# Kernel optimization log

Hardware: AMD Instinct MI355X
Metric: run time of the kernel (lower is better)

The kernel has to match this reference:

```python
import jax, jax.numpy as jnp
import numpy as np

N_NODES = 100000
N_EDGES = 800000
N_DIM = 2
HID = 128
EPS = 1e-12  # torch F.normalize eps


def setup_inputs() -> dict:
    key = jax.random.key(0)
    ks = jax.random.split(key, 12)
    x = jax.random.normal(ks[0], (N_NODES, N_DIM), dtype=jnp.float32)
    v = jax.random.normal(ks[1], (N_NODES, N_DIM), dtype=jnp.float32)
    src = jax.random.randint(ks[2], (N_EDGES,), 0, N_NODES, dtype=jnp.int32)
    dst = jax.random.randint(ks[3], (N_EDGES,), 0, N_NODES, dtype=jnp.int32)
    # fNN parameters, stored as [in, out] (y = h @ W + b, equivalent to torch Linear)
    def lin(k, fan_in, fan_out):
        bound = 1.0 / np.sqrt(fan_in)
        kw, kb = jax.random.split(k)
        W = jax.random.uniform(kw, (fan_in, fan_out), jnp.float32, -bound, bound)
        b = jax.random.uniform(kb, (fan_out,), jnp.float32, -bound, bound)
        return W, b
    W0, b0 = lin(ks[4], 1, HID)
    W1, b1 = lin(ks[5], HID, HID)
    W2, b2 = lin(ks[6], HID, HID)
    W3, b3 = lin(ks[7], HID, 1)
    gamma = jnp.float32(0.1)
    return {"x": x, "v": v, "src": src, "dst": dst, "gamma": gamma,
            "W0": W0, "b0": b0, "W1": W1, "b1": b1,
            "W2": W2, "b2": b2, "W3": W3, "b3": b3}


def reference(x, v, src, dst, gamma, W0, b0, W1, b1, W2, b2, W3, b3):
    n_nodes = x.shape[0]
    # per-edge displacement: dst position - src position (non-periodic euclid)
    dr = x[dst] - x[src]                                  # [E, N_dim]
    abs_dr = jnp.linalg.norm(dr, axis=-1, keepdims=True)  # [E, 1]
    unit_dr = dr / jnp.maximum(abs_dr, EPS)               # F.normalize
    # small MLP on scalar distance: 1 -> 128 -> 128 -> 128 -> 1, ReLU between
    h = jax.nn.relu(abs_dr @ W0 + b0)
    h = jax.nn.relu(h @ W1 + b1)
    h = jax.nn.relu(h @ W2 + b2)
    force = h @ W3 + b3                                   # [E, 1]
    msg = force * unit_dr                                 # [E, N_dim]
    # scatter-sum messages onto destination nodes
    sum_force = jax.ops.segment_sum(msg, dst, num_segments=n_nodes)  # [N, N_dim]
    # acceleration = aggregated force - gamma * velocity
    return sum_force - gamma * v
```

## Files before the change

kernel.cpp:

```cpp
#include <hip/hip_runtime.h>
#include <math.h>


#define M_TAB 2048
#define INV_MTAB (1.0f / 2048.0f)
#define EPSF 1e-12f
#define RANGE_N 2048
#define RSHIFT 11
#define NBUCK 64
#define P_SL 8
#define BCHUNK 2048
#define TPTS 4
#define NTABB (M_TAB / TPTS)
#define MAXRUN 64
#define SRC_BITS 17
#define SRC_MASK 0x1FFFFu

__device__ __forceinline__ void build_table4(
    int base, int tid, const float* __restrict__ W0,
    const float* __restrict__ b0, const float* __restrict__ W1,
    const float* __restrict__ b1, const float* __restrict__ W2,
    const float* __restrict__ b2, const float* __restrict__ W3,
    const float* __restrict__ b3, float* __restrict__ table,
    float* bufA, float* bufB) {
  const int j = tid;
  if (j < 128) {
    float w = W0[j], b = b0[j];
#pragma unroll
    for (int p = 0; p < TPTS; ++p) {
      float u = (float)(base + p) * INV_MTAB;
      float dd = u / (1.f - u);
      bufA[j * TPTS + p] = fmaxf(fmaf(dd, w, b), 0.f);
    }
  }
  __syncthreads();
  float acc[TPTS];
  if (j < 128) {
    float b = b1[j];
#pragma unroll
    for (int p = 0; p < TPTS; ++p) acc[p] = b;
#pragma unroll 8
    for (int k = 0; k < 128; ++k) {
      float w = W1[k * 128 + j];
      float4 h = *(const float4*)&bufA[k * TPTS];
      acc[0] = fmaf(h.x, w, acc[0]);
      acc[1] = fmaf(h.y, w, acc[1]);
      acc[2] = fmaf(h.z, w, acc[2]);
      acc[3] = fmaf(h.w, w, acc[3]);
    }
  }
  __syncthreads();
  if (j < 128) {
#pragma unroll
    for (int p = 0; p < TPTS; ++p) bufB[j * TPTS + p] = fmaxf(acc[p], 0.f);
  }
  __syncthreads();
  if (j < 128) {
    float b = b2[j];
#pragma unroll
    for (int p = 0; p < TPTS; ++p) acc[p] = b;
#pragma unroll 8
    for (int k = 0; k < 128; ++k) {
      float w = W2[k * 128 + j];
      float4 h = *(const float4*)&bufB[k * TPTS];
      acc[0] = fmaf(h.x, w, acc[0]);
      acc[1] = fmaf(h.y, w, acc[1]);
      acc[2] = fmaf(h.z, w, acc[2]);
      acc[3] = fmaf(h.w, w, acc[3]);
    }
    float w3 = W3[j];
#pragma unroll
    for (int p = 0; p < TPTS; ++p) bufA[j * TPTS + p] = fmaxf(acc[p], 0.f) * w3;
  }
  __syncthreads();
  for (int s = 64; s > 0; s >>= 1) {
    if (j < s) {
#pragma unroll
      for (int p = 0; p < TPTS; ++p)
        bufA[j * TPTS + p] += bufA[(j + s) * TPTS + p];
    }
    __syncthreads();
  }
  if (j < TPTS) table[base + j] = bufA[j] + b3[0];
}

__global__ __launch_bounds__(256) void kbin(
    const int* __restrict__ src, const int* __restrict__ dst,
    const float* __restrict__ W0, const float* __restrict__ b0,
    const float* __restrict__ W1, const float* __restrict__ b1,
    const float* __restrict__ W2, const float* __restrict__ b2,
    const float* __restrict__ W3, const float* __restrict__ b3,
    unsigned* __restrict__ binData, int* __restrict__ cntTab,
    int* __restrict__ offTab, float* __restrict__ table, int E, int NB) {
  __shared__ float smem[1024];
  __shared__ int cntL[NBUCK];
  __shared__ int offL[NBUCK];
  const int tid = threadIdx.x;
  const int bid = blockIdx.x;

  if (bid < NTABB) {
    build_table4(bid * TPTS, tid, W0, b0, W1, b1, W2, b2, W3, b3, table,
                 smem, smem + 512);
    return;
  }
  const int b = bid - NTABB;
  if (tid < NBUCK) cntL[tid] = 0;
  __syncthreads();
  const int e0 = b * BCHUNK + tid * 8;
  int mdst[8], msrc[8], mrank[8];
  if (e0 + 7 < E) {
    int4 c0 = *(const int4*)(dst + e0);
    int4 c1 = *(const int4*)(dst + e0 + 4);
    int4 a0 = *(const int4*)(src + e0);
    int4 a1 = *(const int4*)(src + e0 + 4);
    mdst[0] = c0.x; mdst[1] = c0.y; mdst[2] = c0.z; mdst[3] = c0.w;
    mdst[4] = c1.x; mdst[5] = c1.y; mdst[6] = c1.z; mdst[7] = c1.w;
    msrc[0] = a0.x; msrc[1] = a0.y; msrc[2] = a0.z; msrc[3] = a0.w;
    msrc[4] = a1.x; msrc[5] = a1.y; msrc[6] = a1.z; msrc[7] = a1.w;
  } else {
#pragma unroll
    for (int i = 0; i < 8; ++i) {
      bool vv = (e0 + i < E);
      msrc[i] = vv ? src[e0 + i] : 0;
      mdst[i] = vv ? dst[e0 + i] : -1;
    }
  }
#pragma unroll
  for (int i = 0; i < 8; ++i)
    if (mdst[i] >= 0) mrank[i] = atomicAdd(&cntL[mdst[i] >> RSHIFT], 1);
  __syncthreads();
  if (tid == 0) {
    int s = 0;
#pragma unroll
    for (int k = 0; k < NBUCK; ++k) {
      offL[k] = s;
      s += cntL[k];
    }
  }
  __syncthreads();
  if (tid < NBUCK) {
    cntTab[b * NBUCK + tid] = cntL[tid];
    offTab[b * NBUCK + tid] = offL[tid];
  }
  unsigned* gout = binData + (size_t)b * BCHUNK;
#pragma unroll
  for (int i = 0; i < 8; ++i) {
    if (mdst[i] >= 0) {
      int pos = offL[mdst[i] >> RSHIFT] + mrank[i];
      gout[pos] = ((unsigned)(mdst[i] & (RANGE_N - 1)) << SRC_BITS) |
                  (unsigned)msrc[i];
    }
  }
}

__global__ __launch_bounds__(512) void kcons(
    const unsigned* __restrict__ binData, const int* __restrict__ cntTab,
    const int* __restrict__ offTab, const float* __restrict__ table,
    const float* __restrict__ x, float* __restrict__ partial, int NB,
    int n_nodes, int n_out) {
  __shared__ float acc[RANGE_N * 2];
  __shared__ float2 xl[RANGE_N];
  __shared__ int runStart[MAXRUN];
  __shared__ int pref[MAXRUN + 1];
  const int tid = threadIdx.x;
  const int p = blockIdx.x & (P_SL - 1);
  const int r = blockIdx.x >> 3;
  const int node0 = r * RANGE_N;

  for (int i = tid; i < RANGE_N * 2; i += 512) acc[i] = 0.f;
  for (int i = tid; i < RANGE_N; i += 512)
    xl[i] = (node0 + i < n_nodes) ? ((const float2*)x)[node0 + i]
                                  : make_float2(0.f, 0.f);
  const int nrun = (NB - p + P_SL - 1) / P_SL;
  for (int j = tid; j < nrun; j += 512) {
    int b = p + j * P_SL;
    runStart[j] = b * BCHUNK + offTab[b * NBUCK + r];
    pref[j + 1] = cntTab[b * NBUCK + r];
  }
  __syncthreads();
  if (tid == 0) {
    pref[0] = 0;
    for (int j = 0; j < nrun; ++j) pref[j + 1] += pref[j];
  }
  __syncthreads();

  const int T = pref[nrun];
  for (int g = tid; g < T; g += 512) {
    int lo = 0, hi = nrun;
    while (hi - lo > 1) {
      int mid = (lo + hi) >> 1;
      if (pref[mid] <= g) lo = mid; else hi = mid;
    }
    unsigned ent = binData[(size_t)runStart[lo] + (g - pref[lo])];
    int dloc = (int)(ent >> SRC_BITS);
    int s = (int)(ent & SRC_MASK);
    float2 xs = ((const float2*)x)[s];
    float2 xt = xl[dloc];
    float dx = xt.x - xs.x, dy = xt.y - xs.y;
    float d = sqrtf(fmaf(dx, dx, dy * dy));
    float u = d / (1.f + d);
    float idxf = u * (float)M_TAB;
    int i0 = (int)idxf;
    if (i0 > M_TAB - 2) i0 = M_TAB - 2;
    float frac = idxf - (float)i0;
    float f0 = table[i0], f1 = table[i0 + 1];
    float f = fmaf(frac, f1 - f0, f0);
    float sc = f / fmaxf(d, EPSF);
    atomicAdd(&acc[dloc * 2], sc * dx);
    atomicAdd(&acc[dloc * 2 + 1], sc * dy);
  }
  __syncthreads();

  const int cnt2 = min(RANGE_N, n_nodes - node0);
  float2* po = (float2*)(partial + (size_t)p * n_out) + node0;
  const float2* a2 = (const float2*)acc;
  for (int i = tid; i < cnt2; i += 512) po[i] = a2[i];
}

__global__ __launch_bounds__(256) void k4_finish(
    const float4* __restrict__ v4, const float* __restrict__ gamma,
    const float4* __restrict__ part4, float4* __restrict__ out4, int n4) {
  int i = blockIdx.x * blockDim.x + threadIdx.x;
  if (i >= n4) return;
  float g = -gamma[0];
  float4 a = v4[i];
  float4 acc = make_float4(g * a.x, g * a.y, g * a.z, g * a.w);
#pragma unroll
  for (int c = 0; c < P_SL; ++c) {
    float4 p = part4[(size_t)c * n4 + i];
    acc.x += p.x;
    acc.y += p.y;
    acc.z += p.z;
    acc.w += p.w;
  }
  out4[i] = acc;
}

__global__ __launch_bounds__(128) void k2_table(
    const float* __restrict__ W0, const float* __restrict__ b0,
    const float* __restrict__ W1, const float* __restrict__ b1,
    const float* __restrict__ W2, const float* __restrict__ b2,
    const float* __restrict__ W3, const float* __restrict__ b3,
    float* __restrict__ table) {
  __shared__ float bufA[512];
  __shared__ float bufB[512];
  build_table4(blockIdx.x * TPTS, threadIdx.x, W0, b0, W1, b1, W2, b2, W3,
               b3, table, bufA, bufB);
}

__global__ __launch_bounds__(256) void k0_init(const float* __restrict__ v,
                                               const float* __restrict__ gamma,
                                               float* __restrict__ out,
                                               int n) {
  int i = blockIdx.x * blockDim.x + threadIdx.x;
  if (i < n) out[i] = -gamma[0] * v[i];
}

__global__ __launch_bounds__(256) void k3_direct(
    const float* __restrict__ x, const int* __restrict__ src,
    const int* __restrict__ dst, const float* __restrict__ table,
    float* __restrict__ out, int E) {
  int e = blockIdx.x * blockDim.x + threadIdx.x;
  if (e >= E) return;
  int s = src[e], t = dst[e];
  float2 xs = ((const float2*)x)[s];
  float2 xt = ((const float2*)x)[t];
  float dx = xt.x - xs.x, dy = xt.y - xs.y;
  float d = sqrtf(fmaf(dx, dx, dy * dy));
  float u = d / (1.f + d);
  float idxf = u * (float)M_TAB;
  int i0 = (int)idxf;
  if (i0 > M_TAB - 2) i0 = M_TAB - 2;
  float frac = idxf - (float)i0;
  float f = fmaf(frac, table[i0 + 1] - table[i0], table[i0]);
  float sc = f / fmaxf(d, EPSF);
  atomicAdd(&out[2 * t + 0], sc * dx);
  atomicAdd(&out[2 * t + 1], sc * dy);
}

extern "C" void kernel_launch(void* const* d_in, const int* in_sizes, int n_in,
                              void* d_out, int out_size, void* d_ws,
                              size_t ws_size, hipStream_t stream) {
  const float* x = (const float*)d_in[0];
  const float* v = (const float*)d_in[1];
  const int* src = (const int*)d_in[2];
  const int* dst = (const int*)d_in[3];
  const float* gamma = (const float*)d_in[4];
  const float* W0 = (const float*)d_in[5];
  const float* b0 = (const float*)d_in[6];
  const float* W1 = (const float*)d_in[7];
  const float* b1 = (const float*)d_in[8];
  const float* W2 = (const float*)d_in[9];
  const float* b2 = (const float*)d_in[10];
  const float* W3 = (const float*)d_in[11];
  const float* b3 = (const float*)d_in[12];
  float* out = (float*)d_out;
  float* table = (float*)d_ws;

  int n_out = out_size;
  int n_nodes = in_sizes[0] / 2;
  int E = in_sizes[2];

  const int NB = (E + BCHUNK - 1) / BCHUNK;
  const int NR = (n_nodes + RANGE_N - 1) / RANGE_N;
  size_t sz_tab = ((size_t)NB * NBUCK * 4 + 255) & ~(size_t)255;
  size_t off_cnt = 65536;
  size_t off_off = off_cnt + sz_tab;
  size_t off_part = off_off + sz_tab;
  size_t off_bin = off_part + (size_t)P_SL * n_out * 4;
  size_t need = off_bin + (size_t)NB * BCHUNK * 4;

  bool fast = (ws_size >= need) && (n_out == 2 * n_nodes) &&
              (n_nodes <= (1 << SRC_BITS)) && (NR <= NBUCK) &&
              (NB <= P_SL * MAXRUN) && ((n_out & 3) == 0);

  if (fast) {
    int* cntTab = (int*)((char*)d_ws + off_cnt);
    int* offTab = (int*)((char*)d_ws + off_off);
    float* partial = (float*)((char*)d_ws + off_part);
    unsigned* binData = (unsigned*)((char*)d_ws + off_bin);
    hipLaunchKernelGGL(kbin, dim3(NTABB + NB), dim3(256), 0, stream, src, dst,
                       W0, b0, W1, b1, W2, b2, W3, b3, binData, cntTab,
                       offTab, table, E, NB);
    hipLaunchKernelGGL(kcons, dim3(NR * P_SL), dim3(512), 0, stream, binData,
                       cntTab, offTab, table, x, partial, NB, n_nodes, n_out);
    hipLaunchKernelGGL(k4_finish, dim3((n_out / 4 + 255) / 256), dim3(256), 0,
                       stream, (const float4*)v, gamma, (const float4*)partial,
                       (float4*)out, n_out / 4);
  } else {
    hipLaunchKernelGGL(k2_table, dim3(NTABB), dim3(128), 0, stream, W0, b0,
                       W1, b1, W2, b2, W3, b3, table);
    hipLaunchKernelGGL(k0_init, dim3((n_out + 255) / 256), dim3(256), 0,
                       stream, v, gamma, out, n_out);
    hipLaunchKernelGGL(k3_direct, dim3((E + 255) / 256), dim3(256), 0, stream,
                       x, src, dst, table, out, E);
  }
}
```

Before: 38.65 us.

## Fuse final reduction into consumer kernel via last-block counter; halve table points per block

Drops the separate k4_finish launch. Each kcons block now increments a per-range done counter after writing its partial, and the last of the P_SL slices for a range sums all partials and applies -gamma*v directly into the output. kbin resets the counters. Separately, each table-building block now computes 2 points instead of 4, doubling the number of table blocks to spread MLP work across more CUs. This saves one launch and the serial finish pass, at the cost of atomics and fences and a tail where one block per range does the reduction.

```diff
diff --git a/kernel.cpp b/kernel.cpp
--- a/kernel.cpp
+++ b/kernel.cpp
@@ -10,13 +10,13 @@
 #define NBUCK 64
 #define P_SL 8
 #define BCHUNK 2048
-#define TPTS 4
+#define TPTS 2
 #define NTABB (M_TAB / TPTS)
 #define MAXRUN 64
 #define SRC_BITS 17
 #define SRC_MASK 0x1FFFFu
 
-__device__ __forceinline__ void build_table4(
+__device__ __forceinline__ void build_table2(
     int base, int tid, const float* __restrict__ W0,
     const float* __restrict__ b0, const float* __restrict__ W1,
     const float* __restrict__ b1, const float* __restrict__ W2,
@@ -42,11 +42,9 @@
 #pragma unroll 8
     for (int k = 0; k < 128; ++k) {
       float w = W1[k * 128 + j];
-      float4 h = *(const float4*)&bufA[k * TPTS];
+      float2 h = *(const float2*)&bufA[k * TPTS];
       acc[0] = fmaf(h.x, w, acc[0]);
       acc[1] = fmaf(h.y, w, acc[1]);
-      acc[2] = fmaf(h.z, w, acc[2]);
-      acc[3] = fmaf(h.w, w, acc[3]);
     }
   }
   __syncthreads();
@@ -62,11 +60,9 @@
 #pragma unroll 8
     for (int k = 0; k < 128; ++k) {
       float w = W2[k * 128 + j];
-      float4 h = *(const float4*)&bufB[k * TPTS];
+      float2 h = *(const float2*)&bufB[k * TPTS];
       acc[0] = fmaf(h.x, w, acc[0]);
       acc[1] = fmaf(h.y, w, acc[1]);
-      acc[2] = fmaf(h.z, w, acc[2]);
-      acc[3] = fmaf(h.w, w, acc[3]);
     }
     float w3 = W3[j];
 #pragma unroll
@@ -91,19 +87,21 @@
     const float* __restrict__ W2, const float* __restrict__ b2,
     const float* __restrict__ W3, const float* __restrict__ b3,
     unsigned* __restrict__ binData, int* __restrict__ cntTab,
-    int* __restrict__ offTab, float* __restrict__ table, int E, int NB) {
-  __shared__ float smem[1024];
+    int* __restrict__ offTab, float* __restrict__ table,
+    int* __restrict__ done, int E, int NB) {
+  __shared__ float smem[512];
   __shared__ int cntL[NBUCK];
   __shared__ int offL[NBUCK];
   const int tid = threadIdx.x;
   const int bid = blockIdx.x;
 
   if (bid < NTABB) {
-    build_table4(bid * TPTS, tid, W0, b0, W1, b1, W2, b2, W3, b3, table,
-                 smem, smem + 512);
+    build_table2(bid * TPTS, tid, W0, b0, W1, b1, W2, b2, W3, b3, table,
+                 smem, smem + 256);
     return;
   }
   const int b = bid - NTABB;
+  if (b == 0 && tid < NBUCK) done[tid] = 0;
   if (tid < NBUCK) cntL[tid] = 0;
   __syncthreads();
   const int e0 = b * BCHUNK + tid * 8;
@@ -156,12 +154,15 @@
 __global__ __launch_bounds__(512) void kcons(
     const unsigned* __restrict__ binData, const int* __restrict__ cntTab,
     const int* __restrict__ offTab, const float* __restrict__ table,
-    const float* __restrict__ x, float* __restrict__ partial, int NB,
-    int n_nodes, int n_out) {
+    const float* __restrict__ x, const float* __restrict__ v,
+    const float* __restrict__ gamma, float* __restrict__ partial,
+    int* __restrict__ done, float* __restrict__ out, int NB, int n_nodes,
+    int n_out) {
   __shared__ float acc[RANGE_N * 2];
   __shared__ float2 xl[RANGE_N];
   __shared__ int runStart[MAXRUN];
   __shared__ int pref[MAXRUN + 1];
+  __shared__ int isLast;
   const int tid = threadIdx.x;
   const int p = blockIdx.x & (P_SL - 1);
   const int r = blockIdx.x >> 3;
@@ -215,25 +216,31 @@
   float2* po = (float2*)(partial + (size_t)p * n_out) + node0;
   const float2* a2 = (const float2*)acc;
   for (int i = tid; i < cnt2; i += 512) po[i] = a2[i];
-}
-
-__global__ __launch_bounds__(256) void k4_finish(
-    const float4* __restrict__ v4, const float* __restrict__ gamma,
-    const float4* __restrict__ part4, float4* __restrict__ out4, int n4) {
-  int i = blockIdx.x * blockDim.x + threadIdx.x;
-  if (i >= n4) return;
-  float g = -gamma[0];
-  float4 a = v4[i];
-  float4 acc = make_float4(g * a.x, g * a.y, g * a.z, g * a.w);
-#pragma unroll
-  for (int c = 0; c < P_SL; ++c) {
-    float4 p = part4[(size_t)c * n4 + i];
-    acc.x += p.x;
-    acc.y += p.y;
-    acc.z += p.z;
-    acc.w += p.w;
-  }
-  out4[i] = acc;
+
+  __syncthreads();
+  if (tid == 0) {
+    __threadfence();
+    int t = atomicAdd(&done[r], 1);
+    isLast = (t == P_SL - 1);
+  }
+  __syncthreads();
+  if (isLast) {
+    __threadfence();
+    const float gm = -gamma[0];
+    const float2* pv = (const float2*)v + node0;
+    float2* po2 = (float2*)out + node0;
+    for (int i = tid; i < cnt2; i += 512) {
+      float2 s = make_float2(0.f, 0.f);
+#pragma unroll
+      for (int c = 0; c < P_SL; ++c) {
+        float2 pp = ((const float2*)(partial + (size_t)c * n_out))[node0 + i];
+        s.x += pp.x;
+        s.y += pp.y;
+      }
+      float2 vv = pv[i];
+      po2[i] = make_float2(fmaf(gm, vv.x, s.x), fmaf(gm, vv.y, s.y));
+    }
+  }
 }
 
 __global__ __launch_bounds__(128) void k2_table(
@@ -242,9 +249,9 @@
     const float* __restrict__ W2, const float* __restrict__ b2,
     const float* __restrict__ W3, const float* __restrict__ b3,
     float* __restrict__ table) {
-  __shared__ float bufA[512];
-  __shared__ float bufB[512];
-  build_table4(blockIdx.x * TPTS, threadIdx.x, W0, b0, W1, b1, W2, b2, W3,
+  __shared__ float bufA[256];
+  __shared__ float bufB[256];
+  build_table2(blockIdx.x * TPTS, threadIdx.x, W0, b0, W1, b1, W2, b2, W3,
                b3, table, bufA, bufB);
 }
 
@@ -306,7 +313,8 @@
   size_t sz_tab = ((size_t)NB * NBUCK * 4 + 255) & ~(size_t)255;
   size_t off_cnt = 65536;
   size_t off_off = off_cnt + sz_tab;
-  size_t off_part = off_off + sz_tab;
+  size_t off_done = off_off + sz_tab;
+  size_t off_part = off_done + 1024;
   size_t off_bin = off_part + (size_t)P_SL * n_out * 4;
   size_t need = off_bin + (size_t)NB * BCHUNK * 4;
 
@@ -317,16 +325,15 @@
   if (fast) {
     int* cntTab = (int*)((char*)d_ws + off_cnt);
     int* offTab = (int*)((char*)d_ws + off_off);
+    int* done = (int*)((char*)d_ws + off_done);
     float* partial = (float*)((char*)d_ws + off_part);
     unsigned* binData = (unsigned*)((char*)d_ws + off_bin);
     hipLaunchKernelGGL(kbin, dim3(NTABB + NB), dim3(256), 0, stream, src, dst,
                        W0, b0, W1, b1, W2, b2, W3, b3, binData, cntTab,
-                       offTab, table, E, NB);
+                       offTab, table, done, E, NB);
     hipLaunchKernelGGL(kcons, dim3(NR * P_SL), dim3(512), 0, stream, binData,
-                       cntTab, offTab, table, x, partial, NB, n_nodes, n_out);
-    hipLaunchKernelGGL(k4_finish, dim3((n_out / 4 + 255) / 256), dim3(256), 0,
-                       stream, (const float4*)v, gamma, (const float4*)partial,
-                       (float4*)out, n_out / 4);
+                       cntTab, offTab, table, x, v, gamma, partial, done, out,
+                       NB, n_nodes, n_out);
   } else {
     hipLaunchKernelGGL(k2_table, dim3(NTABB), dim3(128), 0, stream, W0, b0,
                        W1, b1, W2, b2, W3, b3, table);
```

New measurement: 116.4 us. +201.2%, slower.
